# Kernel tuning notes

Hardware: AMD Instinct MI355X
Metric: run time of the kernel (lower is better)

## Reference

```python
import jax, jax.numpy as jnp
import numpy as np

NEG_BIG = -9.0e15  # mask value used by the torch module
LEAKY_SLOPE = 0.01  # torch nn.LeakyReLU default


def setup_inputs() -> dict:
    key = jax.random.key(0)
    k1, k2, k3, k4 = jax.random.split(key, 4)
    N, F_in, F_out = 8192, 256, 128
    x = jax.random.normal(k1, (N, F_in), dtype=jnp.float32)
    adj = jax.random.randint(k2, (N, N), 0, 2, dtype=jnp.int32)
    W = jax.random.normal(k3, (F_in, F_out), dtype=jnp.float32) * 0.05
    a = jax.random.normal(k4, (2 * F_out, 1), dtype=jnp.float32) * 0.05
    return {"x": x, "adj": adj, "W": W, "a": a}


def reference(x, adj, W, a):
    F_out = W.shape[1]
    h = x @ W                                   # [N, F_out]
    # e[i, j] = leaky_relu([h_i || h_j] . a) = leaky_relu(h_i.a1 + h_j.a2)
    a1, a2 = a[:F_out, 0], a[F_out:, 0]
    e = h @ a1[:, None] + (h @ a2)[None, :]     # [N, N]
    e = jax.nn.leaky_relu(e, negative_slope=LEAKY_SLOPE)
    scores = jnp.where(adj > 0, e, NEG_BIG)
    attention = jax.nn.softmax(scores, axis=1)  # dropout p=0 -> identity
    h1 = jax.nn.elu(attention @ h)              # [N, F_out]
    return h1, attention
```

## Files before the change

kernel.cpp:

```cpp
#include <hip/hip_runtime.h>

#define N 8192
#define FI 256
#define FO 128

typedef short bf16x8 __attribute__((ext_vector_type(8)));
typedef float f32x4 __attribute__((ext_vector_type(4)));
typedef unsigned short u16x4 __attribute__((ext_vector_type(4)));
typedef unsigned long long u64;
typedef u64 u64x2 __attribute__((ext_vector_type(2)));

static __device__ __forceinline__ unsigned short f2bf(float x) {
  unsigned int u = __builtin_bit_cast(unsigned int, x);
  u = (u + 0x7fffu + ((u >> 16) & 1u)) >> 16;
  return (unsigned short)u;
}
static __device__ __forceinline__ float lrelu(float x) {
  return fmaxf(x, 0.01f * x);
}

__global__ __launch_bounds__(256) void k_prep(
    const float* __restrict__ x, const float* __restrict__ W, const float* __restrict__ a,
    unsigned short* __restrict__ h_t, float* __restrict__ ha1, float* __restrict__ ha2) {
  __shared__ float xs[16][256];
  __shared__ float redA[16][2], redB[16][2];
  const int t = threadIdx.x;
  const int i0 = blockIdx.x * 16;
  #pragma unroll
  for (int ii = 0; ii < 16; ++ii)
    xs[ii][t & 255] = x[(long long)(i0 + ii) * FI + t];
  __syncthreads();
  const int rg = t >> 7;
  const int f = t & 127;
  float accs[8] = {0.f, 0.f, 0.f, 0.f, 0.f, 0.f, 0.f, 0.f};
  for (int k = 0; k < 256; ++k) {
    const float wv = W[k * FO + f];
    #pragma unroll
    for (int rr = 0; rr < 8; ++rr) accs[rr] = fmaf(xs[rg * 8 + rr][k], wv, accs[rr]);
  }
  {
    ushort4 s0, s1;
    s0.x = f2bf(accs[0]); s0.y = f2bf(accs[1]); s0.z = f2bf(accs[2]); s0.w = f2bf(accs[3]);
    s1.x = f2bf(accs[4]); s1.y = f2bf(accs[5]); s1.z = f2bf(accs[6]); s1.w = f2bf(accs[7]);
    unsigned short* dst = h_t + (long long)f * N + i0 + rg * 8;
    *(ushort4*)dst = s0;
    *(ushort4*)(dst + 4) = s1;
  }
  const float a1f = a[f];
  const float a2f = a[FO + f];
  const int lane = t & 63;
  const int wig = (t >> 6) & 1;
  #pragma unroll
  for (int rr = 0; rr < 8; ++rr) {
    float v1 = accs[rr] * a1f;
    float v2 = accs[rr] * a2f;
    #pragma unroll
    for (int off = 32; off; off >>= 1) { v1 += __shfl_xor(v1, off); v2 += __shfl_xor(v2, off); }
    if (lane == 0) { redA[rg * 8 + rr][wig] = v1; redB[rg * 8 + rr][wig] = v2; }
  }
  __syncthreads();
  if (t < 16) {
    ha1[i0 + t] = redA[t][0] + redA[t][1];
    ha2[i0 + t] = redB[t][0] + redB[t][1];
  }
}

template <int WM>
__global__ __launch_bounds__(256) void k_mask(
    const int* __restrict__ adj, const float* __restrict__ ha1g, const float* __restrict__ ha2g,
    u64* __restrict__ msk, float* __restrict__ lse_row) {
  const int t = threadIdx.x;
  const int lane = t & 63;
  const int row = blockIdx.x * 4 + (t >> 6);
  const float ei = ha1g[row];
  const int* __restrict__ arow = adj + (size_t)row * N;
  u64* __restrict__ mrow = msk + (size_t)row * 128;
  float m = -3.0e38f, s = 0.f;
  for (int it = 0; it < 32; ++it) {
    const int j0 = it * 256 + lane * 4;
    const int4 a4 = *(const int4*)(arow + j0);
    const float4 h2 = *(const float4*)(ha2g + j0);
    const bool b0 = a4.x > 0, b1 = a4.y > 0, b2 = a4.z > 0, b3 = a4.w > 0;
    #define ONLINE(bb, vv) { \
      const float t0 = ei + (vv); \
      const float e = lrelu(t0); \
      const float mn = (bb) ? fmaxf(m, e) : m; \
      s = fmaf(s, __expf(m - mn), (bb) ? __expf(e - mn) : 0.f); \
      m = mn; }
    ONLINE(b0, h2.x) ONLINE(b1, h2.y) ONLINE(b2, h2.z) ONLINE(b3, h2.w)
    #undef ONLINE
    if (WM) {
      const u64 q0 = __ballot(b0), q1 = __ballot(b1);
      const u64 q2 = __ballot(b2), q3 = __ballot(b3);
      if (lane == 0) {
        u64x2 v01 = {q0, q1}, v23 = {q2, q3};
        *(u64x2*)(mrow + it * 4) = v01;
        *(u64x2*)(mrow + it * 4 + 2) = v23;
      }
    }
  }
  #pragma unroll
  for (int off = 32; off; off >>= 1) {
    const float mo = __shfl_xor(m, off);
    const float so = __shfl_xor(s, off);
    const float mn = fmaxf(m, mo);
    s = s * __expf(m - mn) + so * __expf(mo - mn);
    m = mn;
  }
  if (lane == 0) lse_row[row] = (s > 0.f) ? (m + __logf(s)) : 3.0e38f;
}

template <int UA>
__global__ __launch_bounds__(512) void k_pv(
    const int* __restrict__ adj, const u64* __restrict__ msk,
    const unsigned short* __restrict__ h_t, const float* __restrict__ ha1g,
    const float* __restrict__ ha2g, const float* __restrict__ lse_row,
    float* __restrict__ h1, float* __restrict__ attn) {
  __shared__ unsigned short p_lds[2][16][136];
  const int t = threadIdx.x;
  const int lane = t & 63;
  const int w = t >> 6;
  const int base = blockIdx.x * 16;
  const int pr = t >> 5;
  const int pjw = t & 31;
  const float ei = ha1g[base + pr];
  const float nls = lse_row[base + pr];
  const u64* __restrict__ mrow = msk + (size_t)(base + pr) * 128;
  const int* __restrict__ arow = adj + (size_t)(base + pr) * N;
  float* __restrict__ atrow = attn + (size_t)(base + pr) * N;

  const int f0 = w * 16;
  const unsigned short* __restrict__ hbase =
      h_t + (size_t)(f0 + (lane & 15)) * N + (lane >> 4) * 8;
  const unsigned short* pfrag0 = &p_lds[0][lane & 15][(lane >> 4) * 8];

  f32x4 acc = {0.f, 0.f, 0.f, 0.f};

  auto compute_p = [&](int jt) {
    const int j = jt * 128 + pjw * 4;
    bool b0, b1, b2, b3;
    if constexpr (UA) {
      const int4 a4 = *(const int4*)(arow + j);
      b0 = a4.x > 0; b1 = a4.y > 0; b2 = a4.z > 0; b3 = a4.w > 0;
    } else {
      const int it = j >> 8;
      const int l = (j >> 2) & 63;
      const u64x2 qa = *(const u64x2*)(mrow + it * 4);
      const u64x2 qb = *(const u64x2*)(mrow + it * 4 + 2);
      b0 = (qa.x >> l) & 1; b1 = (qa.y >> l) & 1;
      b2 = (qb.x >> l) & 1; b3 = (qb.y >> l) & 1;
    }
    const float4 h2 = *(const float4*)(ha2g + j);
    const float p0 = b0 ? __expf(lrelu(ei + h2.x) - nls) : 0.f;
    const float p1 = b1 ? __expf(lrelu(ei + h2.y) - nls) : 0.f;
    const float p2 = b2 ? __expf(lrelu(ei + h2.z) - nls) : 0.f;
    const float p3 = b3 ? __expf(lrelu(ei + h2.w) - nls) : 0.f;
    f32x4 pv = {p0, p1, p2, p3};
    *(f32x4*)(atrow + j) = pv;
    u16x4 pb = {f2bf(p0), f2bf(p1), f2bf(p2), f2bf(p3)};
    *(u16x4*)&p_lds[(jt & 1)][pr][pjw * 4] = pb;
  };

  bf16x8 hA[4], hB[4];
  compute_p(0);
  #pragma unroll
  for (int ks = 0; ks < 4; ++ks) hA[ks] = *(const bf16x8*)(hbase + ks * 32);
  __syncthreads();

  for (int jt = 0; jt < 64; ++jt) {
    if (jt < 63) {
      compute_p(jt + 1);
      #pragma unroll
      for (int ks = 0; ks < 4; ++ks)
        hB[ks] = *(const bf16x8*)(hbase + (jt + 1) * 128 + ks * 32);
    }
    const unsigned short* pf = pfrag0 + (jt & 1) * (16 * 136);
    #pragma unroll
    for (int ks = 0; ks < 4; ++ks) {
      const bf16x8 av = *(const bf16x8*)(pf + ks * 32);
      acc = __builtin_amdgcn_mfma_f32_16x16x32_bf16(av, hA[ks], acc, 0, 0, 0);
    }
    if (jt < 63) {
      __syncthreads();
      #pragma unroll
      for (int ks = 0; ks < 4; ++ks) hA[ks] = hB[ks];
    }
  }
  {
    const int rbase = (lane >> 4) * 4;
    const int col = lane & 15;
    #pragma unroll
    for (int rgi = 0; rgi < 4; ++rgi) {
      float v = acc[rgi];
      v = v > 0.f ? v : __expf(v) - 1.f;
      h1[(long long)(base + rbase + rgi) * FO + f0 + col] = v;
    }
  }
}

extern "C" void kernel_launch(void* const* d_in, const int* in_sizes, int n_in,
                              void* d_out, int out_size, void* d_ws, size_t ws_size,
                              hipStream_t stream) {
  const float* x = (const float*)d_in[0];
  const int* adj = (const int*)d_in[1];
  const float* W = (const float*)d_in[2];
  const float* a = (const float*)d_in[3];
  float* h1 = (float*)d_out;
  float* attn = (float*)d_out + (size_t)N * FO;

  char* wsb = (char*)d_ws;
  unsigned short* h_t = (unsigned short*)wsb;
  float* ha1 = (float*)(wsb + (size_t)FO * N * 2);
  float* ha2 = ha1 + N;
  float* lse = ha2 + N;
  const size_t msk_off = (size_t)FO * N * 2 + 3 * (size_t)N * 4;
  u64* msk = (u64*)(wsb + msk_off);
  const size_t need = msk_off + (size_t)N * 128 * 8;

  k_prep<<<N / 16, 256, 0, stream>>>(x, W, a, h_t, ha1, ha2);
  if (ws_size >= need) {
    k_mask<1><<<N / 4, 256, 0, stream>>>(adj, ha1, ha2, msk, lse);
    k_pv<0><<<N / 16, 512, 0, stream>>>(adj, msk, h_t, ha1, ha2, lse, h1, attn);
  } else {
    k_mask<0><<<N / 4, 256, 0, stream>>>(adj, ha1, ha2, msk, lse);
    k_pv<1><<<N / 16, 512, 0, stream>>>(adj, msk, h_t, ha1, ha2, lse, h1, attn);
  }
}
```

Baseline: 276.1 us.

## Split attention-PV kernel over key halves with partial-sum finalize kernel

The PV/attention kernel now splits the key dimension in two, launching twice as many blocks. Each block writes partial h1 accumulators to workspace, and a new finalize kernel sums the halves and applies ELU. The goal is more parallelism and latency hiding in the memory-bound attention write pass. In exchange it adds extra partial-sum traffic, a kernel launch, and a larger workspace requirement. It also adds an occupancy hint in launch bounds and a scheduling barrier in the loop.

```diff
diff --git a/kernel.cpp b/kernel.cpp
--- a/kernel.cpp
+++ b/kernel.cpp
@@ -110,17 +110,21 @@
   if (lane == 0) lse_row[row] = (s > 0.f) ? (m + __logf(s)) : 3.0e38f;
 }
 
-template <int UA>
-__global__ __launch_bounds__(512) void k_pv(
+template <int UA, int SPLIT>
+__global__ __launch_bounds__(512, 6) void k_pv(
     const int* __restrict__ adj, const u64* __restrict__ msk,
     const unsigned short* __restrict__ h_t, const float* __restrict__ ha1g,
     const float* __restrict__ ha2g, const float* __restrict__ lse_row,
-    float* __restrict__ h1, float* __restrict__ attn) {
+    float* __restrict__ h1, float* __restrict__ attn, float* __restrict__ part) {
   __shared__ unsigned short p_lds[2][16][136];
   const int t = threadIdx.x;
   const int lane = t & 63;
   const int w = t >> 6;
-  const int base = blockIdx.x * 16;
+  const int gb = (SPLIT == 2) ? (blockIdx.x >> 1) : blockIdx.x;
+  const int half = (SPLIT == 2) ? (blockIdx.x & 1) : 0;
+  const int joff = half * (N / SPLIT);
+  const int NIT = (N / SPLIT) / 128;
+  const int base = gb * 16;
   const int pr = t >> 5;
   const int pjw = t & 31;
   const float ei = ha1g[base + pr];
@@ -131,13 +135,13 @@
 
   const int f0 = w * 16;
   const unsigned short* __restrict__ hbase =
-      h_t + (size_t)(f0 + (lane & 15)) * N + (lane >> 4) * 8;
+      h_t + (size_t)(f0 + (lane & 15)) * N + joff + (lane >> 4) * 8;
   const unsigned short* pfrag0 = &p_lds[0][lane & 15][(lane >> 4) * 8];
 
   f32x4 acc = {0.f, 0.f, 0.f, 0.f};
 
   auto compute_p = [&](int jt) {
-    const int j = jt * 128 + pjw * 4;
+    const int j = joff + jt * 128 + pjw * 4;
     bool b0, b1, b2, b3;
     if constexpr (UA) {
       const int4 a4 = *(const int4*)(arow + j);
@@ -167,20 +171,21 @@
   for (int ks = 0; ks < 4; ++ks) hA[ks] = *(const bf16x8*)(hbase + ks * 32);
   __syncthreads();
 
-  for (int jt = 0; jt < 64; ++jt) {
-    if (jt < 63) {
+  for (int jt = 0; jt < NIT; ++jt) {
+    if (jt < NIT - 1) {
       compute_p(jt + 1);
       #pragma unroll
       for (int ks = 0; ks < 4; ++ks)
         hB[ks] = *(const bf16x8*)(hbase + (jt + 1) * 128 + ks * 32);
     }
+    __builtin_amdgcn_sched_barrier(0);
     const unsigned short* pf = pfrag0 + (jt & 1) * (16 * 136);
     #pragma unroll
     for (int ks = 0; ks < 4; ++ks) {
       const bf16x8 av = *(const bf16x8*)(pf + ks * 32);
       acc = __builtin_amdgcn_mfma_f32_16x16x32_bf16(av, hA[ks], acc, 0, 0, 0);
     }
-    if (jt < 63) {
+    if (jt < NIT - 1) {
       __syncthreads();
       #pragma unroll
       for (int ks = 0; ks < 4; ++ks) hA[ks] = hB[ks];
@@ -192,10 +197,33 @@
     #pragma unroll
     for (int rgi = 0; rgi < 4; ++rgi) {
       float v = acc[rgi];
-      v = v > 0.f ? v : __expf(v) - 1.f;
-      h1[(long long)(base + rbase + rgi) * FO + f0 + col] = v;
-    }
-  }
+      if constexpr (SPLIT == 1) {
+        v = v > 0.f ? v : __expf(v) - 1.f;
+        h1[(long long)(base + rbase + rgi) * FO + f0 + col] = v;
+      } else {
+        part[(size_t)blockIdx.x * 2048 + (rbase + rgi) * FO + f0 + col] = v;
+      }
+    }
+  }
+}
+
+__global__ __launch_bounds__(256) void k_fin(
+    const float* __restrict__ part, float* __restrict__ h1) {
+  const int o = (blockIdx.x * 256 + threadIdx.x) * 4;
+  const int i = o >> 7;
+  const int f = o & 127;
+  const int g = i >> 4;
+  const int r = i & 15;
+  const size_t po = (size_t)g * 4096 + r * FO + f;
+  const float4 u0 = *(const float4*)(part + po);
+  const float4 u1 = *(const float4*)(part + po + 2048);
+  float4 v;
+  v.x = u0.x + u1.x; v.y = u0.y + u1.y; v.z = u0.z + u1.z; v.w = u0.w + u1.w;
+  v.x = v.x > 0.f ? v.x : __expf(v.x) - 1.f;
+  v.y = v.y > 0.f ? v.y : __expf(v.y) - 1.f;
+  v.z = v.z > 0.f ? v.z : __expf(v.z) - 1.f;
+  v.w = v.w > 0.f ? v.w : __expf(v.w) - 1.f;
+  *(float4*)(h1 + o) = v;
 }
 
 extern "C" void kernel_launch(void* const* d_in, const int* in_sizes, int n_in,
@@ -215,14 +243,20 @@
   float* lse = ha2 + N;
   const size_t msk_off = (size_t)FO * N * 2 + 3 * (size_t)N * 4;
   u64* msk = (u64*)(wsb + msk_off);
-  const size_t need = msk_off + (size_t)N * 128 * 8;
+  const size_t need_mask = msk_off + (size_t)N * 128 * 8;
+  float* part = (float*)(wsb + need_mask);
+  const size_t need_part = need_mask + (size_t)1024 * 2048 * 4;
 
   k_prep<<<N / 16, 256, 0, stream>>>(x, W, a, h_t, ha1, ha2);
-  if (ws_size >= need) {
+  if (ws_size >= need_part) {
     k_mask<1><<<N / 4, 256, 0, stream>>>(adj, ha1, ha2, msk, lse);
-    k_pv<0><<<N / 16, 512, 0, stream>>>(adj, msk, h_t, ha1, ha2, lse, h1, attn);
+    k_pv<0, 2><<<N / 8, 512, 0, stream>>>(adj, msk, h_t, ha1, ha2, lse, h1, attn, part);
+    k_fin<<<(N * FO) / 1024, 256, 0, stream>>>(part, h1);
+  } else if (ws_size >= need_mask) {
+    k_mask<1><<<N / 4, 256, 0, stream>>>(adj, ha1, ha2, msk, lse);
+    k_pv<0, 1><<<N / 16, 512, 0, stream>>>(adj, msk, h_t, ha1, ha2, lse, h1, attn, part);
   } else {
     k_mask<0><<<N / 4, 256, 0, stream>>>(adj, ha1, ha2, msk, lse);
-    k_pv<1><<<N / 16, 512, 0, stream>>>(adj, msk, h_t, ha1, ha2, lse, h1, attn);
-  }
-}
+    k_pv<1, 1><<<N / 16, 512, 0, stream>>>(adj, msk, h_t, ha1, ha2, lse, h1, attn, part);
+  }
+}
```

Result: no change. 275.7 us (-0.1%).

## Batch eight column tiles per barrier phase in attention-PV kernel

Applied to the files above, without the earlier changes.

The PV kernel now computes probabilities for eight 128-column tiles into an enlarged shared-memory buffer, synchronises once, then runs all MFMAs for those tiles, and synchronises again. This cuts the number of block-wide barriers from one per tile to two per eight tiles, and uses a lighter barrier that waits only on LDS counters. The cost is that the explicit register double-buffering of h_t prefetch is dropped, so global loads of h_t are no longer overlapped with the probability computation. It also uses more LDS per block, which may lower occupancy.

```diff
diff --git a/kernel.cpp b/kernel.cpp
--- a/kernel.cpp
+++ b/kernel.cpp
@@ -17,6 +17,11 @@
 }
 static __device__ __forceinline__ float lrelu(float x) {
   return fmaxf(x, 0.01f * x);
+}
+static __device__ __forceinline__ void barrier_lds() {
+  asm volatile("s_waitcnt lgkmcnt(0)" ::: "memory");
+  __builtin_amdgcn_s_barrier();
+  asm volatile("" ::: "memory");
 }
 
 __global__ __launch_bounds__(256) void k_prep(
@@ -116,7 +121,7 @@
     const unsigned short* __restrict__ h_t, const float* __restrict__ ha1g,
     const float* __restrict__ ha2g, const float* __restrict__ lse_row,
     float* __restrict__ h1, float* __restrict__ attn) {
-  __shared__ unsigned short p_lds[2][16][136];
+  __shared__ unsigned short p_lds[8][16][136];
   const int t = threadIdx.x;
   const int lane = t & 63;
   const int w = t >> 6;
@@ -136,55 +141,46 @@
 
   f32x4 acc = {0.f, 0.f, 0.f, 0.f};
 
-  auto compute_p = [&](int jt) {
-    const int j = jt * 128 + pjw * 4;
-    bool b0, b1, b2, b3;
-    if constexpr (UA) {
-      const int4 a4 = *(const int4*)(arow + j);
-      b0 = a4.x > 0; b1 = a4.y > 0; b2 = a4.z > 0; b3 = a4.w > 0;
-    } else {
-      const int it = j >> 8;
-      const int l = (j >> 2) & 63;
-      const u64x2 qa = *(const u64x2*)(mrow + it * 4);
-      const u64x2 qb = *(const u64x2*)(mrow + it * 4 + 2);
-      b0 = (qa.x >> l) & 1; b1 = (qa.y >> l) & 1;
-      b2 = (qb.x >> l) & 1; b3 = (qb.y >> l) & 1;
-    }
-    const float4 h2 = *(const float4*)(ha2g + j);
-    const float p0 = b0 ? __expf(lrelu(ei + h2.x) - nls) : 0.f;
-    const float p1 = b1 ? __expf(lrelu(ei + h2.y) - nls) : 0.f;
-    const float p2 = b2 ? __expf(lrelu(ei + h2.z) - nls) : 0.f;
-    const float p3 = b3 ? __expf(lrelu(ei + h2.w) - nls) : 0.f;
-    f32x4 pv = {p0, p1, p2, p3};
-    *(f32x4*)(atrow + j) = pv;
-    u16x4 pb = {f2bf(p0), f2bf(p1), f2bf(p2), f2bf(p3)};
-    *(u16x4*)&p_lds[(jt & 1)][pr][pjw * 4] = pb;
-  };
-
-  bf16x8 hA[4], hB[4];
-  compute_p(0);
-  #pragma unroll
-  for (int ks = 0; ks < 4; ++ks) hA[ks] = *(const bf16x8*)(hbase + ks * 32);
-  __syncthreads();
-
-  for (int jt = 0; jt < 64; ++jt) {
-    if (jt < 63) {
-      compute_p(jt + 1);
+  for (int T = 0; T < 8; ++T) {
+    const int jt0 = T * 1024;
+    #pragma unroll
+    for (int s = 0; s < 8; ++s) {
+      const int j = jt0 + s * 128 + pjw * 4;
+      bool b0, b1, b2, b3;
+      if constexpr (UA) {
+        const int4 a4 = *(const int4*)(arow + j);
+        b0 = a4.x > 0; b1 = a4.y > 0; b2 = a4.z > 0; b3 = a4.w > 0;
+      } else {
+        const int it = j >> 8;
+        const int l = (j >> 2) & 63;
+        const u64x2 qa = *(const u64x2*)(mrow + it * 4);
+        const u64x2 qb = *(const u64x2*)(mrow + it * 4 + 2);
+        b0 = (qa.x >> l) & 1; b1 = (qa.y >> l) & 1;
+        b2 = (qb.x >> l) & 1; b3 = (qb.y >> l) & 1;
+      }
+      const float4 h2 = *(const float4*)(ha2g + j);
+      const float p0 = b0 ? __expf(lrelu(ei + h2.x) - nls) : 0.f;
+      const float p1 = b1 ? __expf(lrelu(ei + h2.y) - nls) : 0.f;
+      const float p2 = b2 ? __expf(lrelu(ei + h2.z) - nls) : 0.f;
+      const float p3 = b3 ? __expf(lrelu(ei + h2.w) - nls) : 0.f;
+      f32x4 pv = {p0, p1, p2, p3};
+      *(f32x4*)(atrow + j) = pv;
+      u16x4 pb = {f2bf(p0), f2bf(p1), f2bf(p2), f2bf(p3)};
+      *(u16x4*)&p_lds[s][pr][pjw * 4] = pb;
+    }
+    barrier_lds();
+    #pragma unroll
+    for (int s = 0; s < 8; ++s) {
+      const unsigned short* pf = pfrag0 + s * (16 * 136);
+      const unsigned short* hb = hbase + jt0 + s * 128;
       #pragma unroll
-      for (int ks = 0; ks < 4; ++ks)
-        hB[ks] = *(const bf16x8*)(hbase + (jt + 1) * 128 + ks * 32);
-    }
-    const unsigned short* pf = pfrag0 + (jt & 1) * (16 * 136);
-    #pragma unroll
-    for (int ks = 0; ks < 4; ++ks) {
-      const bf16x8 av = *(const bf16x8*)(pf + ks * 32);
-      acc = __builtin_amdgcn_mfma_f32_16x16x32_bf16(av, hA[ks], acc, 0, 0, 0);
-    }
-    if (jt < 63) {
-      __syncthreads();
-      #pragma unroll
-      for (int ks = 0; ks < 4; ++ks) hA[ks] = hB[ks];
-    }
+      for (int ks = 0; ks < 4; ++ks) {
+        const bf16x8 av = *(const bf16x8*)(pf + ks * 32);
+        const bf16x8 bv = *(const bf16x8*)(hb + ks * 32);
+        acc = __builtin_amdgcn_mfma_f32_16x16x32_bf16(av, bv, acc, 0, 0, 0);
+      }
+    }
+    barrier_lds();
   }
   {
     const int rbase = (lane >> 4) * 4;
```

Result: no change. 278.7 us (+1.0%).
